# Optimization experiments

Hardware: AMD Instinct MI355X
Metric: run time of the kernel (lower is better)

Reference implementation:

```python
import jax, jax.numpy as jnp
import numpy as np

B, S, DIM, HEADS, HEAD_DIM = 4, 1024, 1024, 16, 64
INNER = HEADS * HEAD_DIM
NEG_INF = -1e30


def _rotate_half(t):
    # interleaved pairs: (x1, x2) -> (-x2, x1)
    t = t.reshape(*t.shape[:-1], -1, 2)
    x1, x2 = t[..., 0], t[..., 1]
    return jnp.stack((-x2, x1), axis=-1).reshape(*t.shape[:-2], -1)


def _apply_rope(t, freqs, scale):
    # t: [B, S, INNER]; freqs: [1, S, rot_dim]; rotate only first rot_dim channels
    rot_dim = freqs.shape[-1]
    t_rot, t_pass = t[..., :rot_dim], t[..., rot_dim:]
    t_rot = t_rot * jnp.cos(freqs) * scale + _rotate_half(t_rot) * jnp.sin(freqs) * scale
    return jnp.concatenate((t_rot, t_pass), axis=-1)


def setup_inputs() -> dict:
    key = jax.random.key(0)
    ks = jax.random.split(key, 12)
    x = jax.random.normal(ks[0], (B, S, DIM), dtype=jnp.float32)
    mask = jax.random.bernoulli(ks[1], 0.9, (B, S))
    mask = mask.at[:, 0].set(True)  # ensure every row has a valid key
    # standard rope angles, interleave-repeated to head_dim
    pos = np.arange(S, dtype=np.float32)
    inv_freq = 1.0 / (10000.0 ** (np.arange(0, HEAD_DIM, 2, dtype=np.float32) / HEAD_DIM))
    ang = pos[:, None] * inv_freq[None, :]             # [S, HEAD_DIM//2]
    freqs = jnp.asarray(np.repeat(ang, 2, axis=-1)[None])  # [1, S, HEAD_DIM]
    sc = 1.0 / np.sqrt(DIM)
    def lin(k, din, dout):
        kw, kb = jax.random.split(k)
        return (jax.random.uniform(kw, (din, dout), minval=-sc, maxval=sc),
                jax.random.uniform(kb, (dout,), minval=-sc, maxval=sc))
    Wq, bq = lin(ks[2], DIM, INNER)
    Wk, bk = lin(ks[3], DIM, INNER)
    Wv, bv = lin(ks[4], DIM, INNER)
    Wo, bo = lin(ks[5], INNER, DIM)
    return {"x": x, "mask": mask, "freqs": freqs, "Wq": Wq, "bq": bq,
            "Wk": Wk, "bk": bk, "Wv": Wv, "bv": bv, "Wo": Wo, "bo": bo}


def reference(x, mask, freqs, Wq, bq, Wk, bk, Wv, bv, Wo, bo):
    b = x.shape[0]
    q = x @ Wq + bq
    k = x @ Wk + bk
    v = x @ Wv + bv
    # xpos_scale is None -> scale 1.0 for both q and k
    q = _apply_rope(q, freqs, 1.0)
    k = _apply_rope(k, freqs, 1.0)
    # split heads: [B, H, S, Dh]
    q = q.reshape(b, -1, HEADS, HEAD_DIM).transpose(0, 2, 1, 3)
    k = k.reshape(b, -1, HEADS, HEAD_DIM).transpose(0, 2, 1, 3)
    v = v.reshape(b, -1, HEADS, HEAD_DIM).transpose(0, 2, 1, 3)
    scores = jnp.einsum('bhqd,bhkd->bhqk', q, k) / jnp.sqrt(jnp.float32(HEAD_DIM))
    scores = jnp.where(mask[:, None, None, :], scores, NEG_INF)
    attn = jax.nn.softmax(scores, axis=-1)
    out = jnp.einsum('bhqk,bhkd->bhqd', attn, v)
    out = out.transpose(0, 2, 1, 3).reshape(b, -1, INNER)
    out = out @ Wo + bo
    out = jnp.where(mask[..., None], out, 0.0)
    return out
```

## Files before the change

kernel.cpp:

```cpp
#include <hip/hip_runtime.h>
#include <stdint.h>


typedef unsigned short u16;
typedef __attribute__((ext_vector_type(8))) short short8;
typedef __attribute__((ext_vector_type(4))) float f32x4;
typedef __attribute__((ext_vector_type(4))) unsigned short bf4;

#define LOG2E 1.44269504088896f
#define INV2PI 0.15915494309189535f
#define MFMA_BF16(a,b,c) __builtin_amdgcn_mfma_f32_16x16x32_bf16((a),(b),(c),0,0,0)
#define WAITV(N) asm volatile("s_waitcnt vmcnt(" #N ")" ::: "memory")

__device__ __forceinline__ float bf2f(u16 u){
    union { uint32_t i; float f; } v; v.i = ((uint32_t)u) << 16; return v.f;
}
__device__ __forceinline__ u16 f2bf(float f){
    uint32_t u = __builtin_bit_cast(uint32_t, f);
    u += 0x7FFFu + ((u >> 16) & 1u);
    return (u16)(u >> 16);
}
__device__ __forceinline__ uint32_t cvt_pk_bf16(float lo, float hi){
    uint32_t r;
    asm("v_cvt_pk_bf16_f32 %0, %1, %2" : "=v"(r) : "v"(lo), "v"(hi));
    return r;
}
__device__ __forceinline__ float fast_ex2(float x){
    float r; asm("v_exp_f32 %0, %1" : "=v"(r) : "v"(x)); return r;
}
__device__ __forceinline__ float fast_rcp(float x){
    float r; asm("v_rcp_f32 %0, %1" : "=v"(r) : "v"(x)); return r;
}
__device__ __forceinline__ void fast_sincos(float xrad, float& s, float& c){
    float rev = xrad * INV2PI, fr;
    asm("v_fract_f32 %0, %1" : "=v"(fr) : "v"(rev));
    asm("v_cos_f32 %0, %1" : "=v"(c) : "v"(fr));
    asm("v_sin_f32 %0, %1" : "=v"(s) : "v"(fr));
}

__device__ __forceinline__ void gload_lds16(const void* g, uint32_t dst_lds_byte){
    __builtin_amdgcn_global_load_lds(
        (__attribute__((address_space(1))) uint32_t*)(uintptr_t)g,
        (__attribute__((address_space(3))) uint32_t*)(uintptr_t)dst_lds_byte,
        16, 0, 0);
}

constexpr size_t OFF_XB    = 0;
constexpr size_t OFF_VT    = OFF_XB;
constexpr size_t OFF_WQKVT = 8388608;
constexpr size_t OFF_WOT   = OFF_WQKVT + 6291456;
constexpr size_t OFF_BQKV  = OFF_WOT   + 2097152;
constexpr size_t OFF_MASKB = OFF_BQKV  + 12288;
constexpr size_t OFF_QKV   = OFF_MASKB + 16384;
constexpr size_t OFF_AO    = OFF_QKV   + 25165824;
constexpr size_t WS_NEED   = OFF_AO    + 8388608;

__global__ __launch_bounds__(256) void k_prep(const float* __restrict__ x,
                                              const float* __restrict__ Wq,
                                              const float* __restrict__ Wk,
                                              const float* __restrict__ Wv,
                                              const float* __restrict__ Wo,
                                              const float* __restrict__ bq,
                                              const float* __restrict__ bk,
                                              const float* __restrict__ bv,
                                              const unsigned char* __restrict__ mask,
                                              u16* __restrict__ xb,
                                              u16* __restrict__ Wqkvt,
                                              u16* __restrict__ Wot,
                                              float* __restrict__ bqkv,
                                              float* __restrict__ maskb){
    __shared__ float lds[64][65];
    const int t = threadIdx.x, bid = blockIdx.x;
    if (bid < 4096){
        int gid = bid * 256 + t;
        float4 v = ((const float4*)x)[gid];
        bf4 o;
        o[0] = f2bf(v.x); o[1] = f2bf(v.y); o[2] = f2bf(v.z); o[3] = f2bf(v.w);
        ((bf4*)xb)[gid] = o;
    } else if (bid < 5120){
        int blk = bid - 4096;
        int which = blk >> 8;
        const float* src = which == 0 ? Wq : which == 1 ? Wk : which == 2 ? Wv : Wo;
        u16* dst = which < 3 ? (Wqkvt + (size_t)which * 1024 * 1024) : Wot;
        int n0 = ((blk >> 4) & 15) * 64, k0 = (blk & 15) * 64;
        #pragma unroll
        for (int i = 0; i < 16; i++){
            int idx = t + i * 256; int rr = idx >> 6, cc = idx & 63;
            lds[rr][cc] = src[(size_t)(k0 + rr) * 1024 + n0 + cc];
        }
        __syncthreads();
        #pragma unroll
        for (int i = 0; i < 16; i++){
            int idx = t + i * 256; int rr = idx >> 6, cc = idx & 63;
            dst[(size_t)(n0 + rr) * 1024 + k0 + cc] = f2bf(lds[cc][rr]);
        }
    } else {
        int gid = (bid - 5120) * 256 + t;
        if (gid < 3072){
            bqkv[gid] = gid < 1024 ? bq[gid] : gid < 2048 ? bk[gid - 1024] : bv[gid - 2048];
        } else if (gid < 3072 + 4096){
            int j = gid - 3072;
            int cnt3f = 0;
            #pragma unroll
            for (int i = 0; i < 16; i++) cnt3f += (mask[4 * i + 3] == 0x3F);
            bool v;
            if (cnt3f >= 8){
                v = ((const float*)mask)[j] != 0.f;
            } else {
                int nz = 0;
                for (int i = 1; i < 64; i++) if (i & 3) nz += (mask[i] != 0);
                if (nz) v = mask[j] != 0;
                else    v = ((const int*)mask)[j] != 0;
            }
            maskb[j] = v ? 0.f : -1e30f;
        }
    }
}

__global__ __launch_bounds__(256) void k_gemmq(const u16* __restrict__ A,
                                               const u16* __restrict__ Bt,
                                               const float* __restrict__ bias,
                                               const float* __restrict__ freqs,
                                               u16* __restrict__ Cout){
    constexpr int K = 1024, N = 3072;
    __shared__ alignas(16) u16 sAB[3][2][128 * 32];
    const int t = threadIdx.x;
    const int w = t >> 6, l = t & 63, g = l >> 4, r = l & 15;
    const int brow = blockIdx.x * 128, bcol = blockIdx.y * 128;
    const int wr = (w >> 1) * 64, wc = (w & 1) * 64;
    f32x4 acc[4][4] = {};

    const int lrow = w * 32 + (l >> 2);
    const int lcol = (((l & 3) ^ ((l >> 3) & 3)) * 8);
    const u16* ga = A  + (size_t)(brow + lrow) * K + lcol;
    const u16* gb = Bt + (size_t)(bcol + lrow) * K + lcol;
    const size_t K16 = (size_t)16 * K;
    const uint32_t dst0 = (uint32_t)__builtin_amdgcn_readfirstlane(
        (int)((uint32_t)(uintptr_t)&sAB[0][0][0] + (uint32_t)(w * 2048)));

    constexpr int NT = K >> 5;
    auto stage = [&](int kt, int s){
        const int k0 = kt * 32;
        const uint32_t da = dst0 + (uint32_t)s * 16384;
        gload_lds16(ga + k0,       da);
        gload_lds16(ga + k0 + K16, da + 1024);
        gload_lds16(gb + k0,       da + 8192);
        gload_lds16(gb + k0 + K16, da + 8192 + 1024);
    };

    stage(0, 0);
    stage(1, 1);
    const int rs = (r >> 1) & 3;
    int s_cur = 0;
    for (int kt = 0; kt < NT; ++kt){
        if (kt + 1 < NT) WAITV(4);
        else             WAITV(0);
        __builtin_amdgcn_s_barrier();
        __builtin_amdgcn_sched_barrier(0);
        if (kt + 2 < NT){
            int s_pf = s_cur + 2; if (s_pf >= 3) s_pf -= 3;
            stage(kt + 2, s_pf);
        }
        const u16* sA = &sAB[s_cur][0][0];
        const u16* sB = &sAB[s_cur][1][0];
        short8 af[4], bf[4];
        #pragma unroll
        for (int m = 0; m < 4; m++)
            af[m] = *(const short8*)&sA[(wr + m * 16 + r) * 32 + ((g ^ rs) * 8)];
        #pragma unroll
        for (int n = 0; n < 4; n++)
            bf[n] = *(const short8*)&sB[(wc + n * 16 + r) * 32 + ((g ^ rs) * 8)];
        __builtin_amdgcn_s_setprio(1);
        #pragma unroll
        for (int m = 0; m < 4; m++)
            #pragma unroll
            for (int n = 0; n < 4; n++)
                acc[m][n] = MFMA_BF16(af[m], bf[n], acc[m][n]);
        __builtin_amdgcn_s_setprio(0);
        s_cur = (s_cur == 2) ? 0 : s_cur + 1;
    }

    const bool rope = (bcol == 0 || bcol == 1024) && (wc == 0);
    #pragma unroll
    for (int n = 0; n < 4; n++){
        int col = bcol + wc + n * 16 + r;
        float bb = bias[col];
        float cs = (col < 1024) ? 0.125f : 1.f;
        #pragma unroll
        for (int m = 0; m < 4; m++){
            f32x4 v = acc[m][n];
            #pragma unroll
            for (int jj = 0; jj < 4; jj++){
                int row = brow + wr + m * 16 + g * 4 + jj;
                float val = (v[jj] + bb) * cs;
                if (rope){
                    float partner = __shfl_xor(val, 1);
                    float ang = freqs[(row & 1023) * 64 + (col & 62)];
                    float sn, c;
                    fast_sincos(ang, sn, c);
                    val = (r & 1) ? val * c + partner * sn
                                  : val * c - partner * sn;
                }
                Cout[(size_t)row * N + col] = f2bf(val);
            }
        }
    }
}

__global__ __launch_bounds__(256) void k_gemm_o(const u16* __restrict__ A,
                                                const u16* __restrict__ Bt,
                                                const float* __restrict__ bias,
                                                const float* __restrict__ maskb,
                                                float* __restrict__ Cout){
    constexpr int K = 1024, N = 1024;
    __shared__ alignas(16) u16 sAB[3][6144];
    const int t = threadIdx.x;
    const int w = t >> 6, l = t & 63, g = l >> 4, r = l & 15;
    const int brow = blockIdx.x * 64, bcol = blockIdx.y * 128;
    const int wm = w >> 1, wn = w & 1;
    f32x4 acc[2][4] = {};

    const int lcol = (((l & 3) ^ ((l >> 3) & 3)) * 8);
    const u16* ga = A  + (size_t)(brow + w * 16 + (l >> 2)) * K + lcol;
    const u16* gb = Bt + (size_t)(bcol + w * 32 + (l >> 2)) * K + lcol;
    const size_t K16 = (size_t)16 * K;
    const uint32_t dstA = (uint32_t)__builtin_amdgcn_readfirstlane(
        (int)((uint32_t)(uintptr_t)&sAB[0][0] + (uint32_t)(w * 1024)));
    const uint32_t dstB = (uint32_t)__builtin_amdgcn_readfirstlane(
        (int)((uint32_t)(uintptr_t)&sAB[0][0] + (uint32_t)(4096 + w * 2048)));

    constexpr int NT = K >> 5;
    auto stage = [&](int kt, int s){
        const int k0 = kt * 32;
        const uint32_t off = (uint32_t)s * 12288;
        gload_lds16(ga + k0,       dstA + off);
        gload_lds16(gb + k0,       dstB + off);
        gload_lds16(gb + k0 + K16, dstB + off + 1024);
    };

    stage(0, 0);
    stage(1, 1);
    const int rs = (r >> 1) & 3;
    int s_cur = 0;
    for (int kt = 0; kt < NT; ++kt){
        if (kt + 1 < NT) WAITV(3);
        else             WAITV(0);
        __builtin_amdgcn_s_barrier();
        __builtin_amdgcn_sched_barrier(0);
        if (kt + 2 < NT){
            int s_pf = s_cur + 2; if (s_pf >= 3) s_pf -= 3;
            stage(kt + 2, s_pf);
        }
        const u16* sA = &sAB[s_cur][0];
        const u16* sB = &sAB[s_cur][2048];
        short8 af[2], bf[4];
        #pragma unroll
        for (int m = 0; m < 2; m++)
            af[m] = *(const short8*)&sA[(wm * 32 + m * 16 + r) * 32 + ((g ^ rs) * 8)];
        #pragma unroll
        for (int n = 0; n < 4; n++)
            bf[n] = *(const short8*)&sB[(wn * 64 + n * 16 + r) * 32 + ((g ^ rs) * 8)];
        __builtin_amdgcn_s_setprio(1);
        #pragma unroll
        for (int m = 0; m < 2; m++)
            #pragma unroll
            for (int n = 0; n < 4; n++)
                acc[m][n] = MFMA_BF16(af[m], bf[n], acc[m][n]);
        __builtin_amdgcn_s_setprio(0);
        s_cur = (s_cur == 2) ? 0 : s_cur + 1;
    }

    #pragma unroll
    for (int n = 0; n < 4; n++){
        int col = bcol + wn * 64 + n * 16 + r;
        float bb = bias[col];
        #pragma unroll
        for (int m = 0; m < 2; m++){
            f32x4 v = acc[m][n];
            #pragma unroll
            for (int jj = 0; jj < 4; jj++){
                int row = brow + wm * 32 + m * 16 + g * 4 + jj;
                Cout[(size_t)row * N + col] =
                    (maskb[row] == 0.f) ? (v[jj] + bb) : 0.f;
            }
        }
    }
}

__global__ __launch_bounds__(256) void k_vt(const u16* __restrict__ QKV,
                                            u16* __restrict__ Vt){
    __shared__ u16 lds[64][72];
    const int bh = blockIdx.x >> 4, s0 = (blockIdx.x & 15) * 64;
    const int b = bh >> 4, h = bh & 15;
    const int t = threadIdx.x;
    const u16* src = QKV + (size_t)(b * 1024 + s0) * 3072 + 2048 + h * 64;
    #pragma unroll
    for (int i = 0; i < 2; i++){
        int s = i * 32 + (t >> 3), dc = (t & 7) * 8;
        short8 v = *(const short8*)(src + (size_t)s * 3072 + dc);
        #pragma unroll
        for (int j = 0; j < 8; j++) lds[dc + j][s] = (u16)v[j];
    }
    __syncthreads();
    #pragma unroll
    for (int i = 0; i < 2; i++){
        int d = i * 32 + (t >> 3), sc = (t & 7) * 8;
        short8 v = *(const short8*)&lds[d][sc];
        *(short8*)&Vt[(size_t)(bh * 64 + d) * 1024 + s0 + sc] = v;
    }
}

__global__ __launch_bounds__(256) void k_attn(const u16* __restrict__ QKV,
                                              const u16* __restrict__ Vt,
                                              const float* __restrict__ maskb,
                                              u16* __restrict__ AO){
    __shared__ alignas(16) u16 sK [2][64 * 64];
    __shared__ alignas(16) u16 sVt[2][64 * 64];
    __shared__ alignas(16) u16 sP [4][16 * 64];
    const int t = threadIdx.x, w = t >> 6, l = t & 63, g = l >> 4, r = l & 15;
    const int hw = blockIdx.x;
    const int blk = ((hw & 7) << 7) | (hw >> 3);
    const int qb = blk & 15, h = (blk >> 4) & 15, b = blk >> 8;
    const int bh = b * 16 + h;
    const int qrow0 = b * 1024 + qb * 64 + w * 16;
    const int rx = r & 7;

    const u16* qptr = QKV + (size_t)(qrow0 + r) * 3072 + h * 64;
    short8 qf0 = *(const short8*)(qptr + g * 8);
    short8 qf1 = *(const short8*)(qptr + 32 + g * 8);

    const int srow = l >> 3;
    const int c16  = (l & 7) ^ srow;
    const u16* Kg = QKV + (size_t)(b * 1024) * 3072 + 1024 + h * 64;
    const u16* gK0 = Kg + (size_t)(w * 16 + srow) * 3072 + c16 * 8;
    const u16* gK1 = gK0 + (size_t)8 * 3072;
    const u16* Vg = Vt + (size_t)bh * 64 * 1024;
    const u16* gV0 = Vg + (size_t)(w * 16 + srow) * 1024 + c16 * 8;
    const u16* gV1 = gV0 + (size_t)8 * 1024;
    uint32_t dK0 = (uint32_t)__builtin_amdgcn_readfirstlane(
        (int)((uint32_t)(uintptr_t)&sK[0][0] + (uint32_t)(w * 2048)));
    uint32_t dV0 = (uint32_t)__builtin_amdgcn_readfirstlane(
        (int)((uint32_t)(uintptr_t)&sVt[0][0] + (uint32_t)(w * 2048)));
    char* sPw = (char*)&sP[w][0];
    const char* sKc = (const char*)&sK[0][0];
    const char* sVc = (const char*)&sVt[0][0];

    const float* mkb = maskb + b * 1024;

    f32x4 oacc[4] = {};
    float lsum = 0.f;

    gload_lds16(gK0, dK0);
    gload_lds16(gK1, dK0 + 1024);
    gload_lds16(gV0, dV0);
    gload_lds16(gV1, dV0 + 1024);
    __syncthreads();

    for (int kt = 0; kt < 16; ++kt){
        const int cur = kt & 1;
        if (kt < 15){
            const size_t kv = (size_t)(kt + 1) * 64;
            const uint32_t dk = dK0 + (cur ^ 1) * 8192;
            const uint32_t dv = dV0 + (cur ^ 1) * 8192;
            gload_lds16(gK0 + kv * 3072, dk);
            gload_lds16(gK1 + kv * 3072, dk + 1024);
            gload_lds16(gV0 + kv, dv);
            gload_lds16(gV1 + kv, dv + 1024);
        }
        const char* sKb = sKc + cur * 8192;
        const char* sVb = sVc + cur * 8192;
        const int kv0 = kt * 64;

        f32x4 st[4];
        __builtin_amdgcn_s_setprio(1);
        #pragma unroll
        for (int kn = 0; kn < 4; kn++){
            const int row = kn * 16 + r;
            short8 kf0 = *(const short8*)(sKb + row * 128 + (((g    ) ^ rx) << 4));
            short8 kf1 = *(const short8*)(sKb + row * 128 + (((g + 4) ^ rx) << 4));
            f32x4 z = {};
            z = MFMA_BF16(kf0, qf0, z);
            st[kn] = MFMA_BF16(kf1, qf1, z);
        }
        __builtin_amdgcn_s_setprio(0);

        float p[16];
        #pragma unroll
        for (int kn = 0; kn < 4; kn++){
            f32x4 mbv = *(const f32x4*)(mkb + kv0 + kn * 16 + g * 4);
            #pragma unroll
            for (int jj = 0; jj < 4; jj++){
                float pe = fast_ex2(fmaf(st[kn][jj], LOG2E, mbv[jj]));
                p[kn * 4 + jj] = pe;
                lsum += pe;
            }
        }

        #pragma unroll
        for (int kn = 0; kn < 4; kn++){
            uint2 u;
            u.x = cvt_pk_bf16(p[kn * 4 + 0], p[kn * 4 + 1]);
            u.y = cvt_pk_bf16(p[kn * 4 + 2], p[kn * 4 + 3]);
            *(uint2*)(sPw + r * 128 + ((((2 * kn + (g >> 1))) ^ rx) << 4) + (g & 1) * 8) = u;
        }

        #pragma unroll
        for (int ks = 0; ks < 2; ks++){
            short8 pa = *(const short8*)(sPw + r * 128 + ((((ks << 2) | g) ^ rx) << 4));
            __builtin_amdgcn_s_setprio(1);
            #pragma unroll
            for (int dn = 0; dn < 4; dn++){
                const int vrow = dn * 16 + r;
                short8 vf = *(const short8*)(sVb + vrow * 128 + ((((ks << 2) | g) ^ rx) << 4));
                oacc[dn] = MFMA_BF16(pa, vf, oacc[dn]);
            }
            __builtin_amdgcn_s_setprio(0);
        }
        __syncthreads();
    }

    lsum += __shfl_xor(lsum, 16);
    lsum += __shfl_xor(lsum, 32);
    float linv = fast_rcp(lsum);
    float lf[4];
    #pragma unroll
    for (int jj = 0; jj < 4; jj++) lf[jj] = __shfl(linv, g * 4 + jj);
    #pragma unroll
    for (int dn = 0; dn < 4; dn++)
        #pragma unroll
        for (int jj = 0; jj < 4; jj++)
            AO[(size_t)(qrow0 + g * 4 + jj) * 1024 + h * 64 + dn * 16 + r]
                = f2bf(oacc[dn][jj] * lf[jj]);
}

extern "C" void kernel_launch(void* const* d_in, const int* in_sizes, int n_in,
                              void* d_out, int out_size, void* d_ws, size_t ws_size,
                              hipStream_t stream){
    (void)in_sizes; (void)n_in; (void)out_size;
    if (ws_size < WS_NEED) return;

    const float* x     = (const float*)d_in[0];
    const unsigned char* mask = (const unsigned char*)d_in[1];
    const float* freqs = (const float*)d_in[2];
    const float* Wq    = (const float*)d_in[3];
    const float* bq    = (const float*)d_in[4];
    const float* Wk    = (const float*)d_in[5];
    const float* bk    = (const float*)d_in[6];
    const float* Wv    = (const float*)d_in[7];
    const float* bv    = (const float*)d_in[8];
    const float* Wo    = (const float*)d_in[9];
    const float* bo    = (const float*)d_in[10];

    char* ws = (char*)d_ws;
    u16*   xb    = (u16*)  (ws + OFF_XB);
    u16*   Vtw   = (u16*)  (ws + OFF_VT);
    u16*   Wqkvt = (u16*)  (ws + OFF_WQKVT);
    u16*   Wot   = (u16*)  (ws + OFF_WOT);
    float* bqkv  = (float*)(ws + OFF_BQKV);
    float* maskb = (float*)(ws + OFF_MASKB);
    u16*   QKV   = (u16*)  (ws + OFF_QKV);
    u16*   AO    = (u16*)  (ws + OFF_AO);

    k_prep<<<5148, 256, 0, stream>>>(x, Wq, Wk, Wv, Wo, bq, bk, bv, mask,
                                     xb, Wqkvt, Wot, bqkv, maskb);
    k_gemmq<<<dim3(32, 24), 256, 0, stream>>>(xb, Wqkvt, bqkv, freqs, QKV);
    k_vt   <<<1024, 256, 0, stream>>>(QKV, Vtw);
    k_attn <<<1024, 256, 0, stream>>>(QKV, Vtw, maskb, AO);
    k_gemm_o<<<dim3(64, 8), 256, 0, stream>>>(AO, Wot, bo, maskb, (float*)d_out);
}
```

Before: 110.7 us.

## Rewrite QKV GEMM as 256x256 tile, 8-wave kernel with interleaved staged loads

Replaces the 128x128 four-wave QKV projection GEMM with a 256x256 tile computed by eight waves. It uses 128KB of LDS for double-buffered 64-wide K slices and interleaves partial A/B prefetches between MFMA phases separated by barriers. The aim is more operand reuse per byte loaded and better overlap of global-to-LDS copies with matrix math. The grid shrinks to 192 blocks, fewer than the 256 CUs, so some CUs go idle. The frequent barriers also add synchronisation overhead.

Result: slower. 128.4 us (+16.0%).

```diff
diff --git a/kernel.cpp b/kernel.cpp
--- a/kernel.cpp
+++ b/kernel.cpp
@@ -117,81 +117,142 @@
     }
 }
 
-__global__ __launch_bounds__(256) void k_gemmq(const u16* __restrict__ A,
-                                               const u16* __restrict__ Bt,
-                                               const float* __restrict__ bias,
-                                               const float* __restrict__ freqs,
-                                               u16* __restrict__ Cout){
+__global__ __launch_bounds__(512, 2) void k_gemmq8(const u16* __restrict__ A,
+                                                   const u16* __restrict__ Bt,
+                                                   const float* __restrict__ bias,
+                                                   const float* __restrict__ freqs,
+                                                   u16* __restrict__ Cout){
     constexpr int K = 1024, N = 3072;
-    __shared__ alignas(16) u16 sAB[3][2][128 * 32];
+    __shared__ alignas(16) char lds[131072];
     const int t = threadIdx.x;
     const int w = t >> 6, l = t & 63, g = l >> 4, r = l & 15;
-    const int brow = blockIdx.x * 128, bcol = blockIdx.y * 128;
-    const int wr = (w >> 1) * 64, wc = (w & 1) * 64;
-    f32x4 acc[4][4] = {};
-
-    const int lrow = w * 32 + (l >> 2);
-    const int lcol = (((l & 3) ^ ((l >> 3) & 3)) * 8);
-    const u16* ga = A  + (size_t)(brow + lrow) * K + lcol;
-    const u16* gb = Bt + (size_t)(bcol + lrow) * K + lcol;
-    const size_t K16 = (size_t)16 * K;
-    const uint32_t dst0 = (uint32_t)__builtin_amdgcn_readfirstlane(
-        (int)((uint32_t)(uintptr_t)&sAB[0][0][0] + (uint32_t)(w * 2048)));
-
-    constexpr int NT = K >> 5;
-    auto stage = [&](int kt, int s){
-        const int k0 = kt * 32;
-        const uint32_t da = dst0 + (uint32_t)s * 16384;
-        gload_lds16(ga + k0,       da);
-        gload_lds16(ga + k0 + K16, da + 1024);
-        gload_lds16(gb + k0,       da + 8192);
-        gload_lds16(gb + k0 + K16, da + 8192 + 1024);
+    const int wm = w >> 2, wn = w & 3;
+    const int brow = blockIdx.x * 256, bcol = blockIdx.y * 256;
+    f32x4 acc[8][4] = {};
+
+    const int schunk = (l & 7) ^ (l >> 3);
+    const u16* gA = A  + (size_t)(brow + w * 16 + (l >> 3)) * K + schunk * 8;
+    const u16* gB = Bt + (size_t)(bcol + w * 16 + (l >> 3)) * K + schunk * 8;
+    const size_t R8 = (size_t)8 * K, R128 = (size_t)128 * K;
+    const uint32_t ldsb = (uint32_t)__builtin_amdgcn_readfirstlane(
+        (int)((uint32_t)(uintptr_t)&lds[0] + (uint32_t)(w * 2048)));
+
+    auto stageA = [&](int kt, int h){
+        const uint32_t d = ldsb + (uint32_t)((kt & 1) * 32768 + h * 16384);
+        const u16* s = gA + (size_t)h * R128 + (size_t)(kt * 64);
+        gload_lds16(s,      d);
+        gload_lds16(s + R8, d + 1024);
     };
-
-    stage(0, 0);
-    stage(1, 1);
-    const int rs = (r >> 1) & 3;
-    int s_cur = 0;
-    for (int kt = 0; kt < NT; ++kt){
-        if (kt + 1 < NT) WAITV(4);
-        else             WAITV(0);
-        __builtin_amdgcn_s_barrier();
+    auto stageB = [&](int kt, int h){
+        const uint32_t d = ldsb + (uint32_t)(65536 + (kt & 1) * 32768 + h * 16384);
+        const u16* s = gB + (size_t)h * R128 + (size_t)(kt * 64);
+        gload_lds16(s,      d);
+        gload_lds16(s + R8, d + 1024);
+    };
+
+    const char* ldsA = (const char*)&lds[0];
+    const char* ldsB = (const char*)&lds[65536];
+    const int rx = r & 7;
+
+    stageA(0, 0); stageA(0, 1);
+    stageB(0, 0); stageB(0, 1);
+    stageA(1, 0); stageA(1, 1);
+    WAITV(4);
+    __builtin_amdgcn_s_barrier();
+
+    short8 af[8][2], bf[4][2];
+    for (int kt = 0; kt < 16; ++kt){
+        const int buf = (kt & 1) * 32768;
+        const char* bA = ldsA + buf + (wm * 128 + r) * 128;
+        const char* bB = ldsB + buf + (wn * 64  + r) * 128;
+
+        #pragma unroll
+        for (int m = 0; m < 4; m++)
+            #pragma unroll
+            for (int kk = 0; kk < 2; kk++)
+                af[m][kk] = *(const short8*)(bA + m * 2048 + (((kk * 4 + g) ^ rx) << 4));
+        #pragma unroll
+        for (int n = 0; n < 4; n++)
+            #pragma unroll
+            for (int kk = 0; kk < 2; kk++)
+                bf[n][kk] = *(const short8*)(bB + n * 2048 + (((kk * 4 + g) ^ rx) << 4));
+        if (kt < 15) stageB(kt + 1, 0);
+        __builtin_amdgcn_s_barrier();
+        asm volatile("s_waitcnt lgkmcnt(0)" ::: "memory");
         __builtin_amdgcn_sched_barrier(0);
-        if (kt + 2 < NT){
-            int s_pf = s_cur + 2; if (s_pf >= 3) s_pf -= 3;
-            stage(kt + 2, s_pf);
-        }
-        const u16* sA = &sAB[s_cur][0][0];
-        const u16* sB = &sAB[s_cur][1][0];
-        short8 af[4], bf[4];
-        #pragma unroll
-        for (int m = 0; m < 4; m++)
-            af[m] = *(const short8*)&sA[(wr + m * 16 + r) * 32 + ((g ^ rs) * 8)];
-        #pragma unroll
-        for (int n = 0; n < 4; n++)
-            bf[n] = *(const short8*)&sB[(wc + n * 16 + r) * 32 + ((g ^ rs) * 8)];
         __builtin_amdgcn_s_setprio(1);
         #pragma unroll
-        for (int m = 0; m < 4; m++)
+        for (int m = 0; m < 2; m++)
             #pragma unroll
             for (int n = 0; n < 4; n++)
-                acc[m][n] = MFMA_BF16(af[m], bf[n], acc[m][n]);
+                #pragma unroll
+                for (int kk = 0; kk < 2; kk++)
+                    acc[m][n] = MFMA_BF16(af[m][kk], bf[n][kk], acc[m][n]);
         __builtin_amdgcn_s_setprio(0);
-        s_cur = (s_cur == 2) ? 0 : s_cur + 1;
-    }
-
-    const bool rope = (bcol == 0 || bcol == 1024) && (wc == 0);
+        __builtin_amdgcn_s_barrier();
+
+        #pragma unroll
+        for (int m = 4; m < 8; m++)
+            #pragma unroll
+            for (int kk = 0; kk < 2; kk++)
+                af[m][kk] = *(const short8*)(bA + m * 2048 + (((kk * 4 + g) ^ rx) << 4));
+        if (kt < 15) stageB(kt + 1, 1);
+        __builtin_amdgcn_s_barrier();
+        asm volatile("s_waitcnt lgkmcnt(0)" ::: "memory");
+        __builtin_amdgcn_sched_barrier(0);
+        __builtin_amdgcn_s_setprio(1);
+        #pragma unroll
+        for (int m = 2; m < 4; m++)
+            #pragma unroll
+            for (int n = 0; n < 4; n++)
+                #pragma unroll
+                for (int kk = 0; kk < 2; kk++)
+                    acc[m][n] = MFMA_BF16(af[m][kk], bf[n][kk], acc[m][n]);
+        __builtin_amdgcn_s_setprio(0);
+        __builtin_amdgcn_s_barrier();
+
+        if (kt < 14) stageA(kt + 2, 0);
+        __builtin_amdgcn_s_barrier();
+        __builtin_amdgcn_sched_barrier(0);
+        __builtin_amdgcn_s_setprio(1);
+        #pragma unroll
+        for (int m = 4; m < 6; m++)
+            #pragma unroll
+            for (int n = 0; n < 4; n++)
+                #pragma unroll
+                for (int kk = 0; kk < 2; kk++)
+                    acc[m][n] = MFMA_BF16(af[m][kk], bf[n][kk], acc[m][n]);
+        __builtin_amdgcn_s_setprio(0);
+        __builtin_amdgcn_s_barrier();
+
+        if (kt < 14) stageA(kt + 2, 1);
+        if (kt < 14) { WAITV(4); } else { WAITV(0); }
+        __builtin_amdgcn_s_barrier();
+        __builtin_amdgcn_sched_barrier(0);
+        __builtin_amdgcn_s_setprio(1);
+        #pragma unroll
+        for (int m = 6; m < 8; m++)
+            #pragma unroll
+            for (int n = 0; n < 4; n++)
+                #pragma unroll
+                for (int kk = 0; kk < 2; kk++)
+                    acc[m][n] = MFMA_BF16(af[m][kk], bf[n][kk], acc[m][n]);
+        __builtin_amdgcn_s_setprio(0);
+        __builtin_amdgcn_s_barrier();
+    }
+
+    const bool rope = (bcol == 0 || bcol == 1024) && (wn == 0);
     #pragma unroll
     for (int n = 0; n < 4; n++){
-        int col = bcol + wc + n * 16 + r;
+        int col = bcol + wn * 64 + n * 16 + r;
         float bb = bias[col];
         float cs = (col < 1024) ? 0.125f : 1.f;
         #pragma unroll
-        for (int m = 0; m < 4; m++){
+        for (int m = 0; m < 8; m++){
             f32x4 v = acc[m][n];
             #pragma unroll
             for (int jj = 0; jj < 4; jj++){
-                int row = brow + wr + m * 16 + g * 4 + jj;
+                int row = brow + wm * 128 + m * 16 + g * 4 + jj;
                 float val = (v[jj] + bb) * cs;
                 if (rope){
                     float partner = __shfl_xor(val, 1);
@@ -463,7 +524,7 @@
 
     k_prep<<<5148, 256, 0, stream>>>(x, Wq, Wk, Wv, Wo, bq, bk, bv, mask,
                                      xb, Wqkvt, Wot, bqkv, maskb);
-    k_gemmq<<<dim3(32, 24), 256, 0, stream>>>(xb, Wqkvt, bqkv, freqs, QKV);
+    k_gemmq8<<<dim3(16, 12), 512, 0, stream>>>(xb, Wqkvt, bqkv, freqs, QKV);
     k_vt   <<<1024, 256, 0, stream>>>(QKV, Vtw);
     k_attn <<<1024, 256, 0, stream>>>(QKV, Vtw, maskb, AO);
     k_gemm_o<<<dim3(64, 8), 256, 0, stream>>>(AO, Wot, bo, maskb, (float*)d_out);
```
